# Kernel tuning notes

Hardware: AMD Instinct MI355X
Metric: run time of the kernel (lower is better)

The kernel has to match this reference:

```python
import jax, jax.numpy as jnp
import numpy as np
import math

B, H, S, D = 2, 16, 2048, 128

def setup_inputs() -> dict:
    key = jax.random.key(0)
    kq, kk, kv = jax.random.split(key, 3)
    return {
        "query": jax.random.normal(kq, (B, H, S, D), dtype=jnp.float32),
        "key": jax.random.normal(kk, (B, H, S, D), dtype=jnp.float32),
        "value": jax.random.normal(kv, (B, H, S, D), dtype=jnp.float32),
        "mask": jnp.ones((1, 1, S, S), dtype=jnp.bool_),
    }

def reference(query, key, value, mask):
    # scale_factor=None -> 1/sqrt(head_dim), as in standard SDPA
    head_dim = query.shape[-1]
    scale = 1.0 / math.sqrt(head_dim)
    # [B,H,Sq,Sk] attention scores
    scores = jnp.einsum("bhqd,bhkd->bhqk", query, key) * scale
    neg_inf = jnp.finfo(scores.dtype).min
    scores = jnp.where(mask, scores, neg_inf)
    attn = jax.nn.softmax(scores, axis=-1)  # dropout p=0.0 -> identity
    return jnp.einsum("bhqk,bhkd->bhqd", attn, value)
```

## Files before the change

kernel.cpp:

```cpp
#include <hip/hip_runtime.h>
#include <cstdint>

using short8  = __attribute__((ext_vector_type(8))) short;
using short2v = __attribute__((ext_vector_type(2))) short;
using f32x16  = __attribute__((ext_vector_type(16))) float;
using float4v = __attribute__((ext_vector_type(4))) float;
using int4v   = __attribute__((ext_vector_type(4))) int;

constexpr int Bc = 2, Hc = 16, Sc = 2048, Dc = 128;
constexpr int NW = 4, QBLK = 128, KVBLK = 64;
constexpr int NT = Sc / KVBLK;
constexpr float SCALE_LOG2E = 0.08838834764831845f * 1.4426950408889634f;

__device__ __forceinline__ short f2bf(float f) {
  union { float f; uint32_t u; } v; v.f = f;
  uint32_t u = v.u;
  uint32_t r = (u + 0x7FFFu + ((u >> 16) & 1u)) >> 16;
  return (short)r;
}

__device__ __forceinline__ uint32_t cvtpk(float lo, float hi) {
  uint32_t r;
  asm("v_cvt_pk_bf16_f32 %0, %1, %2" : "=v"(r) : "v"(lo), "v"(hi));
  return r;
}

#define GLOAD_LDS16(g, l)                                                     \
  __builtin_amdgcn_global_load_lds(                                           \
      (const __attribute__((address_space(1))) void*)(g),                     \
      (__attribute__((address_space(3))) void*)(l), 16, 0, 0)

__global__ __launch_bounds__(256)
void conv_k_kernel(const float* __restrict__ K, ushort* __restrict__ Kb) {
  size_t i = ((size_t)blockIdx.x * 256 + threadIdx.x) * 8;
  float4v a = *(const float4v*)(K + i);
  float4v b = *(const float4v*)(K + i + 4);
  short8 r;
  r[0] = f2bf(a[0]); r[1] = f2bf(a[1]); r[2] = f2bf(a[2]); r[3] = f2bf(a[3]);
  r[4] = f2bf(b[0]); r[5] = f2bf(b[1]); r[6] = f2bf(b[2]); r[7] = f2bf(b[3]);
  *(short8*)(Kb + i) = r;
}

__global__ __launch_bounds__(256)
void prep_v_kernel(const float* __restrict__ V, ushort* __restrict__ Vt) {
  __shared__ short T[64 * 66];
  const int bh = blockIdx.y;
  const int st = blockIdx.x & 31, dt = blockIdx.x >> 5;
  const int s0 = st * 64, d0 = dt * 64;
  const float* Vb = V + (size_t)bh * Sc * Dc;
  ushort* Vtb = Vt + (size_t)bh * Dc * Sc;
#pragma unroll
  for (int i = 0; i < 4; ++i) {
    int idx = threadIdx.x + i * 256;
    int r = idx >> 4, c4 = (idx & 15) * 4;
    float4v v = *(const float4v*)&Vb[(size_t)(s0 + r) * Dc + d0 + c4];
    short2v lo, hi;
    lo[0] = f2bf(v[0]); lo[1] = f2bf(v[1]);
    hi[0] = f2bf(v[2]); hi[1] = f2bf(v[3]);
    *(short2v*)&T[r * 66 + c4]     = lo;
    *(short2v*)&T[r * 66 + c4 + 2] = hi;
  }
  __syncthreads();
#pragma unroll
  for (int i = 0; i < 2; ++i) {
    int idx = threadIdx.x + i * 256;
    int dr = idx >> 3, c8 = (idx & 7) * 8;
    short8 o;
#pragma unroll
    for (int j = 0; j < 8; ++j) o[j] = T[(c8 + j) * 66 + dr];
    *(short8*)&Vtb[(size_t)(d0 + dr) * Sc + s0 + c8] = o;
  }
}

__global__ __launch_bounds__(256, 2)
void sdpa_fwd_kernel(const float* __restrict__ Q, const ushort* __restrict__ Kb,
                     const ushort* __restrict__ Vt, float* __restrict__ O) {
  __shared__ __align__(16) short Kl[2][KVBLK * Dc];
  __shared__ __align__(16) short Vl[2][Dc * KVBLK];

  const int tid  = threadIdx.x;
  const int w    = tid >> 6;
  const int lane = tid & 63;
  const int l31  = lane & 31;
  const int hi   = lane >> 5;

  const int bh = blockIdx.x & 31;
  const int qt = blockIdx.x >> 5;
  const size_t base = (size_t)bh * Sc * Dc;
  const float* Qb = Q + base;
  const ushort* KbB = Kb + base;
  const ushort* VtB = Vt + base;

  const int qrow = qt * QBLK + w * 32 + l31;

  short8 qf[8];
#pragma unroll
  for (int c = 0; c < 8; ++c) {
    const float* src = Qb + (size_t)qrow * Dc + c * 16 + hi * 8;
    float4v a = *(const float4v*)src;
    float4v b = *(const float4v*)(src + 4);
    short8 r;
    r[0] = f2bf(a[0] * SCALE_LOG2E); r[1] = f2bf(a[1] * SCALE_LOG2E);
    r[2] = f2bf(a[2] * SCALE_LOG2E); r[3] = f2bf(a[3] * SCALE_LOG2E);
    r[4] = f2bf(b[0] * SCALE_LOG2E); r[5] = f2bf(b[1] * SCALE_LOG2E);
    r[6] = f2bf(b[2] * SCALE_LOG2E); r[7] = f2bf(b[3] * SCALE_LOG2E);
    qf[c] = r;
  }

  int offK[4], offV[4], kldsOff[4], vldsOff[4];
#pragma unroll
  for (int j = 0; j < 4; ++j) {
    int row = w * 16 + j * 4 + (lane >> 4);
    offK[j] = row * Dc + (((lane & 15) ^ (row & 7)) * 8);
    kldsOff[j] = (w * 16 + j * 4) * Dc;
    int d = w * 32 + j * 8 + (lane >> 3);
    offV[j] = d * Sc + (((lane & 7) ^ (d & 7)) * 8);
    vldsOff[j] = (w * 32 + j * 8) * KVBLK;
  }

  auto STAGE = [&](int buf, int kv0) {
#pragma unroll
    for (int j = 0; j < 4; ++j) {
      GLOAD_LDS16(KbB + (size_t)kv0 * Dc + offK[j], &Kl[buf][kldsOff[j]]);
      GLOAD_LDS16(VtB + kv0 + offV[j], &Vl[buf][vldsOff[j]]);
    }
  };

  f32x16 acc[4];
#pragma unroll
  for (int i = 0; i < 4; ++i)
#pragma unroll
    for (int r = 0; r < 16; ++r) acc[i][r] = 0.f;
  float m_run = -1e30f, l_run = 0.f;

  STAGE(0, 0);
  int cur = 0;

  for (int it = 0; it < NT; ++it) {
    __syncthreads();
    if (it + 1 < NT) STAGE(cur ^ 1, (it + 1) * KVBLK);

    f32x16 st[2];
    __builtin_amdgcn_s_setprio(1);
#pragma unroll
    for (int kt = 0; kt < 2; ++kt) {
      f32x16 a;
#pragma unroll
      for (int r = 0; r < 16; ++r) a[r] = 0.f;
#pragma unroll
      for (int c = 0; c < 8; ++c) {
        int elem = ((kt * 32 + l31) * Dc + c * 16 + hi * 8) ^ ((l31 & 7) << 3);
        short8 kf = *(const short8*)&Kl[cur][elem];
        a = __builtin_amdgcn_mfma_f32_32x32x16_bf16(kf, qf[c], a, 0, 0, 0);
      }
      st[kt] = a;
    }
    __builtin_amdgcn_s_setprio(0);

    float t0 = st[0][0], t1 = st[0][1], t2 = st[0][2], t3 = st[0][3];
#pragma unroll
    for (int r = 4; r < 16; r += 4) {
      t0 = fmaxf(t0, st[0][r]);     t1 = fmaxf(t1, st[0][r + 1]);
      t2 = fmaxf(t2, st[0][r + 2]); t3 = fmaxf(t3, st[0][r + 3]);
    }
#pragma unroll
    for (int r = 0; r < 16; r += 4) {
      t0 = fmaxf(t0, st[1][r]);     t1 = fmaxf(t1, st[1][r + 1]);
      t2 = fmaxf(t2, st[1][r + 2]); t3 = fmaxf(t3, st[1][r + 3]);
    }
    float tmax = fmaxf(fmaxf(t0, t1), fmaxf(t2, t3));
    tmax = fmaxf(tmax, __shfl_xor(tmax, 32));

    if (!__all(tmax <= m_run + 8.0f)) {
      float m_new = fmaxf(m_run, tmax);
      float alpha = __builtin_amdgcn_exp2f(m_run - m_new);
      l_run *= alpha;
#pragma unroll
      for (int i = 0; i < 4; ++i)
#pragma unroll
        for (int r = 0; r < 16; ++r) acc[i][r] *= alpha;
      m_run = m_new;
    }

    float ps0 = 0.f, ps1 = 0.f, ps2 = 0.f, ps3 = 0.f;
#pragma unroll
    for (int kt = 0; kt < 2; ++kt)
#pragma unroll
      for (int r = 0; r < 16; r += 4) {
        float p0 = __builtin_amdgcn_exp2f(st[kt][r]     - m_run);
        float p1 = __builtin_amdgcn_exp2f(st[kt][r + 1] - m_run);
        float p2 = __builtin_amdgcn_exp2f(st[kt][r + 2] - m_run);
        float p3 = __builtin_amdgcn_exp2f(st[kt][r + 3] - m_run);
        st[kt][r] = p0; st[kt][r + 1] = p1; st[kt][r + 2] = p2; st[kt][r + 3] = p3;
        ps0 += p0; ps1 += p1; ps2 += p2; ps3 += p3;
      }
    float psum = (ps0 + ps1) + (ps2 + ps3);
    psum += __shfl_xor(psum, 32);
    l_run += psum;

    short8 pf[4];
#pragma unroll
    for (int kc = 0; kc < 4; ++kc) {
      const int kt = kc >> 1;
      const int g0 = (2 * kc) & 3, g1 = (2 * kc + 1) & 3;
      uint32_t a0 = cvtpk(st[kt][4 * g0 + 0], st[kt][4 * g0 + 1]);
      uint32_t b0 = cvtpk(st[kt][4 * g1 + 0], st[kt][4 * g1 + 1]);
      asm volatile("v_permlane32_swap_b32 %0, %1" : "+v"(a0), "+v"(b0));
      uint32_t a1 = cvtpk(st[kt][4 * g0 + 2], st[kt][4 * g0 + 3]);
      uint32_t b1 = cvtpk(st[kt][4 * g1 + 2], st[kt][4 * g1 + 3]);
      asm volatile("v_permlane32_swap_b32 %0, %1" : "+v"(a1), "+v"(b1));
      int4v wv; wv[0] = (int)a0; wv[1] = (int)a1; wv[2] = (int)b0; wv[3] = (int)b1;
      union { int4v i; short8 s; } u; u.i = wv;
      pf[kc] = u.s;
    }

    __builtin_amdgcn_s_setprio(1);
#pragma unroll
    for (int kc = 0; kc < 4; ++kc) {
#pragma unroll
      for (int dt = 0; dt < 4; ++dt) {
        int d = dt * 32 + l31;
        int elem = (d * KVBLK + kc * 16 + hi * 8) ^ ((l31 & 7) << 3);
        short8 vf = *(const short8*)&Vl[cur][elem];
        acc[dt] = __builtin_amdgcn_mfma_f32_32x32x16_bf16(vf, pf[kc], acc[dt], 0, 0, 0);
      }
    }
    __builtin_amdgcn_s_setprio(0);
    cur ^= 1;
  }

  const float inv_l = 1.0f / l_run;
  float* Ob = O + base + (size_t)qrow * Dc;
#pragma unroll
  for (int dt = 0; dt < 4; ++dt)
#pragma unroll
    for (int g = 0; g < 4; ++g) {
      float4v o;
      o[0] = acc[dt][4 * g + 0] * inv_l; o[1] = acc[dt][4 * g + 1] * inv_l;
      o[2] = acc[dt][4 * g + 2] * inv_l; o[3] = acc[dt][4 * g + 3] * inv_l;
      *(float4v*)&Ob[dt * 32 + 8 * g + 4 * hi] = o;
    }
}

extern "C" void kernel_launch(void* const* d_in, const int* in_sizes, int n_in,
                              void* d_out, int out_size, void* d_ws, size_t ws_size,
                              hipStream_t stream) {
  const float* Q = (const float*)d_in[0];
  const float* K = (const float*)d_in[1];
  const float* V = (const float*)d_in[2];
  float* O = (float*)d_out;

  const size_t nElem = (size_t)Bc * Hc * Sc * Dc;
  ushort* Kb = (ushort*)d_ws;
  ushort* Vt = Kb + nElem;

  conv_k_kernel<<<dim3(nElem / (256 * 8)), dim3(256), 0, stream>>>(K, Kb);
  prep_v_kernel<<<dim3(64, Bc * Hc), dim3(256), 0, stream>>>(V, Vt);

  sdpa_fwd_kernel<<<dim3((Sc / QBLK) * Bc * Hc), dim3(256), 0, stream>>>(Q, Kb, Vt, O);
}
```

Measured before the change: 103.6 us.

## Widen attention blocks to 8 waves and 128-key stages; merge prep kernels

The attention kernel now runs 512 threads (8 waves) per block covering 256 query rows. Each stage loads 128 keys and values into LDS, processed as two 64-key sub-steps, so each staged K/V tile is reused by twice as many queries and the per-stage barriers are amortized. The K conversion and V transpose kernels are merged into one launch to cut launch overhead. LDS use per block doubles to 128 KB, and the grid drops to 256 blocks, which may limit occupancy and leave CUs underused on a 256-CU part.

```diff
diff --git a/kernel.cpp b/kernel.cpp
--- a/kernel.cpp
+++ b/kernel.cpp
@@ -8,8 +8,9 @@
 using int4v   = __attribute__((ext_vector_type(4))) int;
 
 constexpr int Bc = 2, Hc = 16, Sc = 2048, Dc = 128;
-constexpr int NW = 4, QBLK = 128, KVBLK = 64;
-constexpr int NT = Sc / KVBLK;
+constexpr int NW = 8, QBLK = 256;
+constexpr int KVS = 128;
+constexpr int NT = Sc / KVS;
 constexpr float SCALE_LOG2E = 0.08838834764831845f * 1.4426950408889634f;
 
 __device__ __forceinline__ short f2bf(float f) {
@@ -31,21 +32,23 @@
       (__attribute__((address_space(3))) void*)(l), 16, 0, 0)
 
 __global__ __launch_bounds__(256)
-void conv_k_kernel(const float* __restrict__ K, ushort* __restrict__ Kb) {
-  size_t i = ((size_t)blockIdx.x * 256 + threadIdx.x) * 8;
-  float4v a = *(const float4v*)(K + i);
-  float4v b = *(const float4v*)(K + i + 4);
-  short8 r;
-  r[0] = f2bf(a[0]); r[1] = f2bf(a[1]); r[2] = f2bf(a[2]); r[3] = f2bf(a[3]);
-  r[4] = f2bf(b[0]); r[5] = f2bf(b[1]); r[6] = f2bf(b[2]); r[7] = f2bf(b[3]);
-  *(short8*)(Kb + i) = r;
-}
-
-__global__ __launch_bounds__(256)
-void prep_v_kernel(const float* __restrict__ V, ushort* __restrict__ Vt) {
+void prep_kernel(const float* __restrict__ K, const float* __restrict__ V,
+                 ushort* __restrict__ Kb, ushort* __restrict__ Vt) {
   __shared__ short T[64 * 66];
-  const int bh = blockIdx.y;
-  const int st = blockIdx.x & 31, dt = blockIdx.x >> 5;
+  if (blockIdx.x < 4096) {
+    size_t i = ((size_t)blockIdx.x * 256 + threadIdx.x) * 8;
+    float4v a = *(const float4v*)(K + i);
+    float4v b = *(const float4v*)(K + i + 4);
+    short8 r;
+    r[0] = f2bf(a[0]); r[1] = f2bf(a[1]); r[2] = f2bf(a[2]); r[3] = f2bf(a[3]);
+    r[4] = f2bf(b[0]); r[5] = f2bf(b[1]); r[6] = f2bf(b[2]); r[7] = f2bf(b[3]);
+    *(short8*)(Kb + i) = r;
+    return;
+  }
+  const int pid = blockIdx.x - 4096;
+  const int bh = pid >> 6;
+  const int xy = pid & 63;
+  const int st = xy & 31, dt = xy >> 5;
   const int s0 = st * 64, d0 = dt * 64;
   const float* Vb = V + (size_t)bh * Sc * Dc;
   ushort* Vtb = Vt + (size_t)bh * Dc * Sc;
@@ -72,11 +75,11 @@
   }
 }
 
-__global__ __launch_bounds__(256, 2)
+__global__ __launch_bounds__(512, 2)
 void sdpa_fwd_kernel(const float* __restrict__ Q, const ushort* __restrict__ Kb,
                      const ushort* __restrict__ Vt, float* __restrict__ O) {
-  __shared__ __align__(16) short Kl[2][KVBLK * Dc];
-  __shared__ __align__(16) short Vl[2][Dc * KVBLK];
+  __shared__ __align__(16) short Kl[2][KVS * Dc];
+  __shared__ __align__(16) short Vl[2][Dc * KVS];
 
   const int tid  = threadIdx.x;
   const int w    = tid >> 6;
@@ -113,9 +116,9 @@
     int row = w * 16 + j * 4 + (lane >> 4);
     offK[j] = row * Dc + (((lane & 15) ^ (row & 7)) * 8);
     kldsOff[j] = (w * 16 + j * 4) * Dc;
-    int d = w * 32 + j * 8 + (lane >> 3);
-    offV[j] = d * Sc + (((lane & 7) ^ (d & 7)) * 8);
-    vldsOff[j] = (w * 32 + j * 8) * KVBLK;
+    int d = w * 16 + j * 4 + (lane >> 4);
+    offV[j] = d * Sc + (((lane & 15) ^ (d & 7)) * 8);
+    vldsOff[j] = (w * 16 + j * 4) * KVS;
   }
 
   auto STAGE = [&](int buf, int kv0) {
@@ -138,94 +141,99 @@
 
   for (int it = 0; it < NT; ++it) {
     __syncthreads();
-    if (it + 1 < NT) STAGE(cur ^ 1, (it + 1) * KVBLK);
-
-    f32x16 st[2];
-    __builtin_amdgcn_s_setprio(1);
-#pragma unroll
-    for (int kt = 0; kt < 2; ++kt) {
-      f32x16 a;
-#pragma unroll
-      for (int r = 0; r < 16; ++r) a[r] = 0.f;
-#pragma unroll
-      for (int c = 0; c < 8; ++c) {
-        int elem = ((kt * 32 + l31) * Dc + c * 16 + hi * 8) ^ ((l31 & 7) << 3);
-        short8 kf = *(const short8*)&Kl[cur][elem];
-        a = __builtin_amdgcn_mfma_f32_32x32x16_bf16(kf, qf[c], a, 0, 0, 0);
-      }
-      st[kt] = a;
+    if (it + 1 < NT) STAGE(cur ^ 1, (it + 1) * KVS);
+
+#pragma unroll
+    for (int sub = 0; sub < 2; ++sub) {
+      f32x16 st[2];
+      __builtin_amdgcn_s_setprio(1);
+#pragma unroll
+      for (int kt = 0; kt < 2; ++kt) {
+        f32x16 a;
+#pragma unroll
+        for (int r = 0; r < 16; ++r) a[r] = 0.f;
+#pragma unroll
+        for (int c = 0; c < 8; ++c) {
+          int elem = ((sub * 64 + kt * 32 + l31) * Dc + c * 16 + hi * 8) ^
+                     ((l31 & 7) << 3);
+          short8 kf = *(const short8*)&Kl[cur][elem];
+          a = __builtin_amdgcn_mfma_f32_32x32x16_bf16(kf, qf[c], a, 0, 0, 0);
+        }
+        st[kt] = a;
+      }
+      __builtin_amdgcn_s_setprio(0);
+
+      float t0 = st[0][0], t1 = st[0][1], t2 = st[0][2], t3 = st[0][3];
+#pragma unroll
+      for (int r = 4; r < 16; r += 4) {
+        t0 = fmaxf(t0, st[0][r]);     t1 = fmaxf(t1, st[0][r + 1]);
+        t2 = fmaxf(t2, st[0][r + 2]); t3 = fmaxf(t3, st[0][r + 3]);
+      }
+#pragma unroll
+      for (int r = 0; r < 16; r += 4) {
+        t0 = fmaxf(t0, st[1][r]);     t1 = fmaxf(t1, st[1][r + 1]);
+        t2 = fmaxf(t2, st[1][r + 2]); t3 = fmaxf(t3, st[1][r + 3]);
+      }
+      float tmax = fmaxf(fmaxf(t0, t1), fmaxf(t2, t3));
+      tmax = fmaxf(tmax, __shfl_xor(tmax, 32));
+
+      if (!__all(tmax <= m_run + 8.0f)) {
+        float m_new = fmaxf(m_run, tmax);
+        float alpha = __builtin_amdgcn_exp2f(m_run - m_new);
+        l_run *= alpha;
+#pragma unroll
+        for (int i = 0; i < 4; ++i)
+#pragma unroll
+          for (int r = 0; r < 16; ++r) acc[i][r] *= alpha;
+        m_run = m_new;
+      }
+
+      float ps0 = 0.f, ps1 = 0.f, ps2 = 0.f, ps3 = 0.f;
+#pragma unroll
+      for (int kt = 0; kt < 2; ++kt)
+#pragma unroll
+        for (int r = 0; r < 16; r += 4) {
+          float p0 = __builtin_amdgcn_exp2f(st[kt][r]     - m_run);
+          float p1 = __builtin_amdgcn_exp2f(st[kt][r + 1] - m_run);
+          float p2 = __builtin_amdgcn_exp2f(st[kt][r + 2] - m_run);
+          float p3 = __builtin_amdgcn_exp2f(st[kt][r + 3] - m_run);
+          st[kt][r] = p0; st[kt][r + 1] = p1;
+          st[kt][r + 2] = p2; st[kt][r + 3] = p3;
+          ps0 += p0; ps1 += p1; ps2 += p2; ps3 += p3;
+        }
+      float psum = (ps0 + ps1) + (ps2 + ps3);
+      psum += __shfl_xor(psum, 32);
+      l_run += psum;
+
+      short8 pf[4];
+#pragma unroll
+      for (int kc = 0; kc < 4; ++kc) {
+        const int kt = kc >> 1;
+        const int g0 = (2 * kc) & 3, g1 = (2 * kc + 1) & 3;
+        uint32_t a0 = cvtpk(st[kt][4 * g0 + 0], st[kt][4 * g0 + 1]);
+        uint32_t b0 = cvtpk(st[kt][4 * g1 + 0], st[kt][4 * g1 + 1]);
+        asm volatile("v_permlane32_swap_b32 %0, %1" : "+v"(a0), "+v"(b0));
+        uint32_t a1 = cvtpk(st[kt][4 * g0 + 2], st[kt][4 * g0 + 3]);
+        uint32_t b1 = cvtpk(st[kt][4 * g1 + 2], st[kt][4 * g1 + 3]);
+        asm volatile("v_permlane32_swap_b32 %0, %1" : "+v"(a1), "+v"(b1));
+        int4v wv; wv[0] = (int)a0; wv[1] = (int)a1; wv[2] = (int)b0; wv[3] = (int)b1;
+        union { int4v i; short8 s; } u; u.i = wv;
+        pf[kc] = u.s;
+      }
+
+      __builtin_amdgcn_s_setprio(1);
+#pragma unroll
+      for (int kc = 0; kc < 4; ++kc) {
+#pragma unroll
+        for (int dt = 0; dt < 4; ++dt) {
+          int d = dt * 32 + l31;
+          int elem = (d * KVS + sub * 64 + kc * 16 + hi * 8) ^ ((l31 & 7) << 3);
+          short8 vf = *(const short8*)&Vl[cur][elem];
+          acc[dt] = __builtin_amdgcn_mfma_f32_32x32x16_bf16(vf, pf[kc], acc[dt], 0, 0, 0);
+        }
+      }
+      __builtin_amdgcn_s_setprio(0);
     }
-    __builtin_amdgcn_s_setprio(0);
-
-    float t0 = st[0][0], t1 = st[0][1], t2 = st[0][2], t3 = st[0][3];
-#pragma unroll
-    for (int r = 4; r < 16; r += 4) {
-      t0 = fmaxf(t0, st[0][r]);     t1 = fmaxf(t1, st[0][r + 1]);
-      t2 = fmaxf(t2, st[0][r + 2]); t3 = fmaxf(t3, st[0][r + 3]);
-    }
-#pragma unroll
-    for (int r = 0; r < 16; r += 4) {
-      t0 = fmaxf(t0, st[1][r]);     t1 = fmaxf(t1, st[1][r + 1]);
-      t2 = fmaxf(t2, st[1][r + 2]); t3 = fmaxf(t3, st[1][r + 3]);
-    }
-    float tmax = fmaxf(fmaxf(t0, t1), fmaxf(t2, t3));
-    tmax = fmaxf(tmax, __shfl_xor(tmax, 32));
-
-    if (!__all(tmax <= m_run + 8.0f)) {
-      float m_new = fmaxf(m_run, tmax);
-      float alpha = __builtin_amdgcn_exp2f(m_run - m_new);
-      l_run *= alpha;
-#pragma unroll
-      for (int i = 0; i < 4; ++i)
-#pragma unroll
-        for (int r = 0; r < 16; ++r) acc[i][r] *= alpha;
-      m_run = m_new;
-    }
-
-    float ps0 = 0.f, ps1 = 0.f, ps2 = 0.f, ps3 = 0.f;
-#pragma unroll
-    for (int kt = 0; kt < 2; ++kt)
-#pragma unroll
-      for (int r = 0; r < 16; r += 4) {
-        float p0 = __builtin_amdgcn_exp2f(st[kt][r]     - m_run);
-        float p1 = __builtin_amdgcn_exp2f(st[kt][r + 1] - m_run);
-        float p2 = __builtin_amdgcn_exp2f(st[kt][r + 2] - m_run);
-        float p3 = __builtin_amdgcn_exp2f(st[kt][r + 3] - m_run);
-        st[kt][r] = p0; st[kt][r + 1] = p1; st[kt][r + 2] = p2; st[kt][r + 3] = p3;
-        ps0 += p0; ps1 += p1; ps2 += p2; ps3 += p3;
-      }
-    float psum = (ps0 + ps1) + (ps2 + ps3);
-    psum += __shfl_xor(psum, 32);
-    l_run += psum;
-
-    short8 pf[4];
-#pragma unroll
-    for (int kc = 0; kc < 4; ++kc) {
-      const int kt = kc >> 1;
-      const int g0 = (2 * kc) & 3, g1 = (2 * kc + 1) & 3;
-      uint32_t a0 = cvtpk(st[kt][4 * g0 + 0], st[kt][4 * g0 + 1]);
-      uint32_t b0 = cvtpk(st[kt][4 * g1 + 0], st[kt][4 * g1 + 1]);
-      asm volatile("v_permlane32_swap_b32 %0, %1" : "+v"(a0), "+v"(b0));
-      uint32_t a1 = cvtpk(st[kt][4 * g0 + 2], st[kt][4 * g0 + 3]);
-      uint32_t b1 = cvtpk(st[kt][4 * g1 + 2], st[kt][4 * g1 + 3]);
-      asm volatile("v_permlane32_swap_b32 %0, %1" : "+v"(a1), "+v"(b1));
-      int4v wv; wv[0] = (int)a0; wv[1] = (int)a1; wv[2] = (int)b0; wv[3] = (int)b1;
-      union { int4v i; short8 s; } u; u.i = wv;
-      pf[kc] = u.s;
-    }
-
-    __builtin_amdgcn_s_setprio(1);
-#pragma unroll
-    for (int kc = 0; kc < 4; ++kc) {
-#pragma unroll
-      for (int dt = 0; dt < 4; ++dt) {
-        int d = dt * 32 + l31;
-        int elem = (d * KVBLK + kc * 16 + hi * 8) ^ ((l31 & 7) << 3);
-        short8 vf = *(const short8*)&Vl[cur][elem];
-        acc[dt] = __builtin_amdgcn_mfma_f32_32x32x16_bf16(vf, pf[kc], acc[dt], 0, 0, 0);
-      }
-    }
-    __builtin_amdgcn_s_setprio(0);
     cur ^= 1;
   }
 
@@ -254,8 +262,7 @@
   ushort* Kb = (ushort*)d_ws;
   ushort* Vt = Kb + nElem;
 
-  conv_k_kernel<<<dim3(nElem / (256 * 8)), dim3(256), 0, stream>>>(K, Kb);
-  prep_v_kernel<<<dim3(64, Bc * Hc), dim3(256), 0, stream>>>(V, Vt);
-
-  sdpa_fwd_kernel<<<dim3((Sc / QBLK) * Bc * Hc), dim3(256), 0, stream>>>(Q, Kb, Vt, O);
-}
+  prep_kernel<<<dim3(4096 + 64 * Bc * Hc), dim3(256), 0, stream>>>(K, V, Kb, Vt);
+
+  sdpa_fwd_kernel<<<dim3((Sc / QBLK) * Bc * Hc), dim3(512), 0, stream>>>(Q, Kb, Vt, O);
+}
```

Measured after the change: 99.42 us. 1.04x faster.
